# Optimization experiments

Hardware: AMD Instinct MI355X
Metric: run time of the kernel (lower is better)

Reference implementation:

```python
import jax, jax.numpy as jnp
import numpy as np

NUM_HEADS = 16
EMB = 1024
HEAD = 64
SEQ = 2048
BATCH = 4


def setup_inputs() -> dict:
    key = jax.random.key(0)
    ks = jax.random.split(key, 6)
    s = EMB ** -0.5
    x = jax.random.normal(ks[0], (BATCH, SEQ, EMB), dtype=jnp.float32)
    # per-head projection weights stacked: [H, E, D] (Linear(emb, head, bias=False) per head)
    Wq = jax.random.normal(ks[1], (NUM_HEADS, EMB, HEAD), dtype=jnp.float32) * s
    Wk = jax.random.normal(ks[2], (NUM_HEADS, EMB, HEAD), dtype=jnp.float32) * s
    Wv = jax.random.normal(ks[3], (NUM_HEADS, EMB, HEAD), dtype=jnp.float32) * s
    # output projection Linear(head*num_heads, emb): weight [E, H*D], bias [E]
    Wo = jax.random.normal(ks[4], (EMB, NUM_HEADS * HEAD), dtype=jnp.float32) * ((NUM_HEADS * HEAD) ** -0.5)
    bo = jax.random.normal(ks[5], (EMB,), dtype=jnp.float32) * 0.01
    return {"x": x, "Wq": Wq, "Wk": Wk, "Wv": Wv, "Wo": Wo, "bo": bo}


def reference(x, Wq, Wk, Wv, Wo, bo):
    B, S, E = x.shape
    scale = HEAD ** -0.5
    # batched per-head projections: [B, H, S, D]
    q = jnp.einsum('bse,hed->bhsd', x, Wq)
    k = jnp.einsum('bse,hed->bhsd', x, Wk)
    v = jnp.einsum('bse,hed->bhsd', x, Wv)
    scores = jnp.einsum('bhqd,bhkd->bhqk', q, k) * scale
    causal = jnp.tril(jnp.ones((S, S), dtype=bool))
    scores = jnp.where(causal, scores, jnp.finfo(scores.dtype).min)
    attn = jax.nn.softmax(scores, axis=-1)  # dropout disabled (eval/deterministic)
    ctx = jnp.einsum('bhqk,bhkd->bhqd', attn, v)
    # concat heads along last dim (head-major order, matching torch.cat)
    concat = ctx.transpose(0, 2, 1, 3).reshape(B, S, NUM_HEADS * HEAD)
    out = concat @ Wo.T + bo
    return out
```

## Files before the change

kernel.cpp:

```cpp
#include <hip/hip_runtime.h>

#define NHEADS 16
#define EMB 1024
#define HDIM 64
#define SEQ 2048
#define BATCH 4

typedef unsigned short u16;
typedef __attribute__((ext_vector_type(8))) __bf16 bf16x8;
typedef __attribute__((ext_vector_type(4))) float f32x4;

#if __has_builtin(__builtin_amdgcn_exp2f)
#define EXP2(x) __builtin_amdgcn_exp2f(x)
#else
#define EXP2(x) __expf((x)*0.69314718056f)
#endif
#define CL2E 0.18033688011112042f

#define BARRIER() __builtin_amdgcn_s_barrier()
#define SB0() __builtin_amdgcn_sched_barrier(0)
#define PRIO1() __builtin_amdgcn_s_setprio(1)
#define PRIO0() __builtin_amdgcn_s_setprio(0)
#define VMCNT(n) asm volatile("s_waitcnt vmcnt(" #n ")" ::: "memory")
#define LGKM0() asm volatile("s_waitcnt lgkmcnt(0)" ::: "memory")

__device__ __forceinline__ u16 f2bf(float f) {
  union { float f; unsigned u; } v; v.f = f;
  unsigned r = v.u + 0x7fffu + ((v.u >> 16) & 1u);
  return (u16)(r >> 16);
}
__device__ __forceinline__ unsigned pk2bf(float a, float b) {
  union { __bf16 h[2]; unsigned u; } x;
  x.h[0] = (__bf16)a; x.h[1] = (__bf16)b; return x.u;
}
__device__ __forceinline__ void gl16(const void* g, void* l) {
  __builtin_amdgcn_global_load_lds(
      (const __attribute__((address_space(1))) unsigned*)g,
      (__attribute__((address_space(3))) unsigned*)l, 16, 0, 0);
}
__device__ __forceinline__ unsigned PKLO(unsigned a, unsigned b) {
  return __builtin_amdgcn_perm(a, b, 0x01000504u);
}
__device__ __forceinline__ unsigned PKHI(unsigned a, unsigned b) {
  return __builtin_amdgcn_perm(a, b, 0x03020706u);
}

__global__ __launch_bounds__(256) void k_cvt(const float* __restrict__ in,
                                             u16* __restrict__ out, int n4) {
  int i = blockIdx.x * 256 + threadIdx.x;
  if (i >= n4) return;
  f32x4 v = *(const f32x4*)(in + (size_t)i * 4);
  uint2 o;
  o.x = (unsigned)f2bf(v[0]) | ((unsigned)f2bf(v[1]) << 16);
  o.y = (unsigned)f2bf(v[2]) | ((unsigned)f2bf(v[3]) << 16);
  *(uint2*)(out + (size_t)i * 4) = o;
}

__global__ __launch_bounds__(256) void k_packw(const float* __restrict__ Wq,
                                               const float* __restrict__ Wk,
                                               const float* __restrict__ Wv,
                                               u16* __restrict__ Wt) {
  const int mh = blockIdx.x;
  const int e0 = blockIdx.y * 64;
  const int mtx = mh >> 4, h = mh & 15;
  const float* W = (mtx == 0 ? Wq : (mtx == 1 ? Wk : Wv)) + (size_t)h * EMB * HDIM;
  __shared__ u16 sT[64][65];
  const int t = threadIdx.x;
  {
    int e = t >> 2, d0 = (t & 3) * 16;
#pragma unroll
    for (int jj = 0; jj < 4; jj++) {
      f32x4 v = *(const f32x4*)(W + (size_t)(e0 + e) * HDIM + d0 + jj * 4);
#pragma unroll
      for (int kk = 0; kk < 4; kk++) sT[e][d0 + jj * 4 + kk] = f2bf(v[kk]);
    }
  }
  __syncthreads();
  {
    int d = t >> 2, eb = (t & 3) * 16;
#pragma unroll
    for (int j = 0; j < 16; j++)
      Wt[(size_t)(mh * 64 + d) * EMB + e0 + eb + j] = sT[eb + j][d];
  }
}

__global__ __launch_bounds__(512, 2) void k_gemm_qkv8(const u16* __restrict__ Xb,
                                                      const u16* __restrict__ Wt,
                                                      u16* __restrict__ Q,
                                                      u16* __restrict__ K,
                                                      u16* __restrict__ V) {
  extern __shared__ __align__(16) char smem[];
  const int bid = blockIdx.x;
  const int l = (bid & 7) * 64 + (bid >> 3);
  const int mt = l & 31, nt = l >> 5;
  const int m0 = mt * 256, n0 = nt * 192;

  const int t = threadIdx.x;
  const int wave = t >> 6, lane = t & 63, lr = lane & 15, lg = lane >> 4;
  const int wr = (wave >> 2) * 128;
  const int wc = (wave & 3) * 48;

  const f32x4 fz = {0.f, 0.f, 0.f, 0.f};
  f32x4 acc[8][3];
#pragma unroll
  for (int i = 0; i < 8; i++)
#pragma unroll
    for (int j = 0; j < 3; j++) acc[i][j] = fz;

  bf16x8 af[4][2], bfr[3][2];

  auto SROUND = [&](char* ldsbase, int rbase, const u16* src, int gRowBase, int kt) {
    int rs = rbase + wave * 8;
    int row = rs + (lane >> 3);
    int gc = (lane & 7) ^ (row & 7);
    gl16(src + (size_t)(gRowBase + row) * EMB + kt * 64 + gc * 8, ldsbase + rs * 128);
  };
  auto STAGE7 = [&](char* nA, char* nB, int kt) {
    SROUND(nB, 0, Wt, n0, kt); SROUND(nB, 64, Wt, n0, kt); SROUND(nB, 128, Wt, n0, kt);
    SROUND(nA, 0, Xb, m0, kt); SROUND(nA, 64, Xb, m0, kt);
    SROUND(nA, 128, Xb, m0, kt); SROUND(nA, 192, Xb, m0, kt);
  };
  auto LOADA = [&](const char* bA, int mh) {
#pragma unroll
    for (int mf = 0; mf < 4; mf++)
#pragma unroll
      for (int kf = 0; kf < 2; kf++) {
        int row = wr + mh * 64 + mf * 16 + lr;
        af[mf][kf] = *(const bf16x8*)(bA + row * 128 + ((kf * 64 + lg * 16) ^ ((row & 7) << 4)));
      }
  };
  auto LOADB = [&](const char* bB) {
#pragma unroll
    for (int nf = 0; nf < 3; nf++)
#pragma unroll
      for (int kf = 0; kf < 2; kf++) {
        int row = wc + nf * 16 + lr;
        bfr[nf][kf] = *(const bf16x8*)(bB + row * 128 + ((kf * 64 + lg * 16) ^ ((row & 7) << 4)));
      }
  };

#define MFMAPH(MH)                                                                         \
  do {                                                                                     \
    _Pragma("unroll") for (int kf = 0; kf < 2; kf++)                                       \
    _Pragma("unroll") for (int mf = 0; mf < 4; mf++)                                       \
    _Pragma("unroll") for (int nf = 0; nf < 3; nf++)                                       \
      acc[(MH)*4 + mf][nf] = __builtin_amdgcn_mfma_f32_16x16x32_bf16(                      \
          af[mf][kf], bfr[nf][kf], acc[(MH)*4 + mf][nf], 0, 0, 0);                         \
  } while (0)

  const int NT = EMB / 64;
  STAGE7(smem, smem + 32768, 0);
  VMCNT(0);
  BARRIER();

  for (int tt = 0; tt < NT - 1; tt++) {
    const int cb = tt & 1, nb = cb ^ 1;
    char* bA = smem + cb * 57344;
    char* bB = bA + 32768;
    char* nA = smem + nb * 57344;
    char* nB = nA + 32768;
    STAGE7(nA, nB, tt + 1);
    VMCNT(7);
    BARRIER(); SB0();
    LOADA(bA, 0);
    LOADB(bB);
    PRIO1(); MFMAPH(0); PRIO0();
    LOADA(bA, 1);
    PRIO1(); MFMAPH(1); PRIO0();
    BARRIER();
  }
  {
    char* bA = smem + ((NT - 1) & 1) * 57344;
    char* bB = bA + 32768;
    VMCNT(0);
    BARRIER(); SB0();
    LOADA(bA, 0);
    LOADB(bB);
    PRIO1(); MFMAPH(0); PRIO0();
    LOADA(bA, 1);
    PRIO1(); MFMAPH(1); PRIO0();
  }
#undef MFMAPH

  const int b = m0 >> 11;
  const int s0 = m0 & 2047;
#pragma unroll
  for (int am = 0; am < 8; am++)
#pragma unroll
    for (int nf = 0; nf < 3; nf++)
#pragma unroll
      for (int r = 0; r < 4; r++) {
        int row = wr + am * 16 + lg * 4 + r;
        int n = n0 + wc + nf * 16 + lr;
        int mtx = n >> 10, h = (n >> 6) & 15, d = n & 63;
        u16* dst = (mtx == 0 ? Q : (mtx == 1 ? K : V));
        dst[((size_t)(b * NHEADS + h) * SEQ + s0 + row) * HDIM + d] = f2bf(acc[am][nf][r]);
      }
}

__global__ __launch_bounds__(256, 3) void k_attn(const u16* __restrict__ Q,
                                                 const u16* __restrict__ K,
                                                 const u16* __restrict__ V,
                                                 u16* __restrict__ Cc) {
  const int bh = blockIdx.x;
  const int qt = 15 - (int)blockIdx.y;
  const int b = bh >> 4, h = bh & 15;
  const int t = threadIdx.x;
  const int wq = t >> 6, lane = t & 63, lr = lane & 15, lg = lane >> 4;
  const size_t base = (size_t)bh * SEQ * HDIM;

  __shared__ __align__(16) char sK[2][64 * 128];
  __shared__ __align__(16) char sV[2][64 * 128];
  __shared__ __align__(16) char sP[128 * 128];

  const int kvb = (t & 15) * 4, db = (t >> 4) * 4;
  uint2 v0, v1, v2, v3;
  auto VLOAD = [&](int k0) {
    const u16* vp = V + base + (size_t)(k0 + kvb) * HDIM + db;
    v0 = *(const uint2*)(vp);
    v1 = *(const uint2*)(vp + HDIM);
    v2 = *(const uint2*)(vp + 2 * HDIM);
    v3 = *(const uint2*)(vp + 3 * HDIM);
  };
  auto VWRITE = [&](char* sv) {
    uint2 w0 = {PKLO(v0.x, v1.x), PKLO(v2.x, v3.x)};
    uint2 w1 = {PKHI(v0.x, v1.x), PKHI(v2.x, v3.x)};
    uint2 w2 = {PKLO(v0.y, v1.y), PKLO(v2.y, v3.y)};
    uint2 w3 = {PKHI(v0.y, v1.y), PKHI(v2.y, v3.y)};
    *(uint2*)(sv + (db + 0) * 128 + ((kvb * 2) ^ (((db + 0) & 7) << 4))) = w0;
    *(uint2*)(sv + (db + 1) * 128 + ((kvb * 2) ^ (((db + 1) & 7) << 4))) = w1;
    *(uint2*)(sv + (db + 2) * 128 + ((kvb * 2) ^ (((db + 2) & 7) << 4))) = w2;
    *(uint2*)(sv + (db + 3) * 128 + ((kvb * 2) ^ (((db + 3) & 7) << 4))) = w3;
  };
  auto KSTAGE = [&](char* sk, int k0) {
#pragma unroll
    for (int i = 0; i < 2; i++) {
      int rb = wq * 16 + i * 8;
      int row = rb + (lane >> 3);
      int gc = (lane & 7) ^ (row & 7);
      gl16(K + base + (size_t)(k0 + row) * HDIM + gc * 8, sk + rb * 128);
    }
  };

#pragma unroll
  for (int i = 0; i < 4; i++) {
    int rb = wq * 32 + i * 8;
    int row = rb + (lane >> 3);
    int gc = (lane & 7) ^ (row & 7);
    gl16(Q + base + (size_t)(qt * 128 + row) * HDIM + gc * 8, sP + rb * 128);
  }
  KSTAGE(sK[0], 0);
  VLOAD(0);
  VMCNT(0);
  VWRITE(sV[0]);
  __syncthreads();

  bf16x8 qf[2][2];
#pragma unroll
  for (int q2 = 0; q2 < 2; q2++)
#pragma unroll
    for (int kf = 0; kf < 2; kf++) {
      int row = wq * 32 + q2 * 16 + lr;
      qf[q2][kf] = *(const bf16x8*)(sP + row * 128 + ((kf * 64 + lg * 16) ^ ((row & 7) << 4)));
    }

  const f32x4 fz = {0.f, 0.f, 0.f, 0.f};
  f32x4 ot[4][2];
#pragma unroll
  for (int df = 0; df < 4; df++)
#pragma unroll
    for (int q2 = 0; q2 < 2; q2++) ot[df][q2] = fz;
  float m_[2] = {-1e30f, -1e30f}, l_[2] = {0.f, 0.f};

  const int nsteps = 2 * qt + 2;
  for (int step = 0; step < nsteps; step++) {
    const int k0 = step * 64;
    const int cur = step & 1, nxt = cur ^ 1;
    const bool pf = (step + 1 < nsteps);
    if (pf) {
      KSTAGE(sK[nxt], k0 + 64);
      VLOAD(k0 + 64);
    }

    f32x4 st[4][2];
#pragma unroll
    for (int kvf = 0; kvf < 4; kvf++)
#pragma unroll
      for (int q2 = 0; q2 < 2; q2++) st[kvf][q2] = fz;
#pragma unroll
    for (int kf = 0; kf < 2; kf++) {
      bf16x8 kfr[4];
#pragma unroll
      for (int kvf = 0; kvf < 4; kvf++) {
        int row = kvf * 16 + lr;
        kfr[kvf] = *(const bf16x8*)(sK[cur] + row * 128 + ((kf * 64 + lg * 16) ^ ((row & 7) << 4)));
      }
      PRIO1();
#pragma unroll
      for (int kvf = 0; kvf < 4; kvf++)
#pragma unroll
        for (int q2 = 0; q2 < 2; q2++)
          st[kvf][q2] = __builtin_amdgcn_mfma_f32_16x16x32_bf16(kfr[kvf], qf[q2][kf], st[kvf][q2], 0, 0, 0);
      PRIO0();
    }

    const bool diag = (k0 >= qt * 128);
    float mxv[2];
#pragma unroll
    for (int q2 = 0; q2 < 2; q2++) {
      if (diag) {
        const int qg = qt * 128 + wq * 32 + q2 * 16 + lr;
#pragma unroll
        for (int kvf = 0; kvf < 4; kvf++)
#pragma unroll
          for (int r = 0; r < 4; r++)
            if (k0 + kvf * 16 + 4 * lg + r > qg) st[kvf][q2][r] = -3e38f;
      }
      float mx = -3e38f;
#pragma unroll
      for (int kvf = 0; kvf < 4; kvf++)
        mx = fmaxf(mx, fmaxf(fmaxf(st[kvf][q2][0], st[kvf][q2][1]),
                             fmaxf(st[kvf][q2][2], st[kvf][q2][3])));
      mx = fmaxf(mx, __shfl_xor(mx, 16));
      mx = fmaxf(mx, __shfl_xor(mx, 32));
      mxv[q2] = mx;
    }
    if (!__all((mxv[0] <= m_[0] + 64.f) && (mxv[1] <= m_[1] + 64.f))) {
#pragma unroll
      for (int q2 = 0; q2 < 2; q2++) {
        float mnew = fmaxf(m_[q2], mxv[q2]);
        float alpha = EXP2((m_[q2] - mnew) * CL2E);
        m_[q2] = mnew;
        l_[q2] *= alpha;
#pragma unroll
        for (int df = 0; df < 4; df++) ot[df][q2] *= alpha;
      }
    }
#pragma unroll
    for (int q2 = 0; q2 < 2; q2++) {
      float nmc = -m_[q2] * CL2E;
      float rs = 0.f;
      const int prow = wq * 32 + q2 * 16 + lr;
#pragma unroll
      for (int kvf = 0; kvf < 4; kvf++) {
        float p0 = EXP2(fmaf(st[kvf][q2][0], CL2E, nmc));
        float p1 = EXP2(fmaf(st[kvf][q2][1], CL2E, nmc));
        float p2 = EXP2(fmaf(st[kvf][q2][2], CL2E, nmc));
        float p3 = EXP2(fmaf(st[kvf][q2][3], CL2E, nmc));
        rs += (p0 + p1) + (p2 + p3);
        uint2 w;
        w.x = pk2bf(p0, p1);
        w.y = pk2bf(p2, p3);
        *(uint2*)(sP + prow * 128 + ((kvf * 32 + lg * 8) ^ ((prow & 7) << 4))) = w;
      }
      rs += __shfl_xor(rs, 16);
      rs += __shfl_xor(rs, 32);
      l_[q2] += rs;
    }

#pragma unroll
    for (int kf = 0; kf < 2; kf++) {
      bf16x8 pfg[2], vf[4];
#pragma unroll
      for (int q2 = 0; q2 < 2; q2++) {
        int row = wq * 32 + q2 * 16 + lr;
        pfg[q2] = *(const bf16x8*)(sP + row * 128 + ((kf * 64 + lg * 16) ^ ((row & 7) << 4)));
      }
#pragma unroll
      for (int df = 0; df < 4; df++) {
        int row = df * 16 + lr;
        vf[df] = *(const bf16x8*)(sV[cur] + row * 128 + ((kf * 64 + lg * 16) ^ ((row & 7) << 4)));
      }
      PRIO1();
#pragma unroll
      for (int df = 0; df < 4; df++)
#pragma unroll
        for (int q2 = 0; q2 < 2; q2++)
          ot[df][q2] = __builtin_amdgcn_mfma_f32_16x16x32_bf16(vf[df], pfg[q2], ot[df][q2], 0, 0, 0);
      PRIO0();
    }

    if (pf) {
      VMCNT(0);
      VWRITE(sV[nxt]);
      LGKM0();
      BARRIER();
    }
  }

#pragma unroll
  for (int q2 = 0; q2 < 2; q2++) {
    float inv = 1.0f / l_[q2];
    int s = qt * 128 + wq * 32 + q2 * 16 + lr;
#pragma unroll
    for (int df = 0; df < 4; df++) {
      uint2 w;
      w.x = pk2bf(ot[df][q2][0] * inv, ot[df][q2][1] * inv);
      w.y = pk2bf(ot[df][q2][2] * inv, ot[df][q2][3] * inv);
      *(uint2*)(Cc + ((size_t)b * SEQ + s) * (NHEADS * HDIM) + h * HDIM + df * 16 + 4 * lg) = w;
    }
  }
}

__global__ __launch_bounds__(512, 2) void k_gemm_out8(const u16* __restrict__ Cc,
                                                      const u16* __restrict__ Wob,
                                                      const float* __restrict__ bo,
                                                      float* __restrict__ out) {
  extern __shared__ __align__(16) char smem[];
  const int bid = blockIdx.x;
  const int l = (bid & 7) * 32 + (bid >> 3);
  const int mt = l & 31, nt = l >> 5;
  const int m0 = mt * 256, n0 = nt * 128;

  const int t = threadIdx.x;
  const int wave = t >> 6, lane = t & 63, lr = lane & 15, lg = lane >> 4;
  const int wr = (wave >> 2) * 128;
  const int wc = (wave & 3) * 32;

  const f32x4 fz = {0.f, 0.f, 0.f, 0.f};
  f32x4 acc[8][2];
#pragma unroll
  for (int i = 0; i < 8; i++)
#pragma unroll
    for (int j = 0; j < 2; j++) acc[i][j] = fz;

  bf16x8 af[4][2], bfr[2][2];

  auto SROUND = [&](char* ldsbase, int rbase, const u16* src, int gRowBase, int kt) {
    int rs = rbase + wave * 8;
    int row = rs + (lane >> 3);
    int gc = (lane & 7) ^ (row & 7);
    gl16(src + (size_t)(gRowBase + row) * EMB + kt * 64 + gc * 8, ldsbase + rs * 128);
  };
  auto STAGE6 = [&](char* nA, char* nB, int kt) {
    SROUND(nB, 0, Wob, n0, kt); SROUND(nB, 64, Wob, n0, kt);
    SROUND(nA, 0, Cc, m0, kt); SROUND(nA, 64, Cc, m0, kt);
    SROUND(nA, 128, Cc, m0, kt); SROUND(nA, 192, Cc, m0, kt);
  };
  auto LOADA = [&](const char* bA, int mh) {
#pragma unroll
    for (int mf = 0; mf < 4; mf++)
#pragma unroll
      for (int kf = 0; kf < 2; kf++) {
        int row = wr + mh * 64 + mf * 16 + lr;
        af[mf][kf] = *(const bf16x8*)(bA + row * 128 + ((kf * 64 + lg * 16) ^ ((row & 7) << 4)));
      }
  };
  auto LOADB = [&](const char* bB) {
#pragma unroll
    for (int nf = 0; nf < 2; nf++)
#pragma unroll
      for (int kf = 0; kf < 2; kf++) {
        int row = wc + nf * 16 + lr;
        bfr[nf][kf] = *(const bf16x8*)(bB + row * 128 + ((kf * 64 + lg * 16) ^ ((row & 7) << 4)));
      }
  };

#define MFMAPH2(MH)                                                                        \
  do {                                                                                     \
    _Pragma("unroll") for (int kf = 0; kf < 2; kf++)                                       \
    _Pragma("unroll") for (int mf = 0; mf < 4; mf++)                                       \
    _Pragma("unroll") for (int nf = 0; nf < 2; nf++)                                       \
      acc[(MH)*4 + mf][nf] = __builtin_amdgcn_mfma_f32_16x16x32_bf16(                      \
          af[mf][kf], bfr[nf][kf], acc[(MH)*4 + mf][nf], 0, 0, 0);                         \
  } while (0)

  const int NT = EMB / 64;
  STAGE6(smem, smem + 32768, 0);
  VMCNT(0);
  BARRIER();

  for (int tt = 0; tt < NT - 1; tt++) {
    const int cb = tt & 1, nb = cb ^ 1;
    char* bA = smem + cb * 49152;
    char* bB = bA + 32768;
    char* nA = smem + nb * 49152;
    char* nB = nA + 32768;
    STAGE6(nA, nB, tt + 1);
    VMCNT(6);
    BARRIER(); SB0();
    LOADA(bA, 0);
    LOADB(bB);
    PRIO1(); MFMAPH2(0); PRIO0();
    LOADA(bA, 1);
    PRIO1(); MFMAPH2(1); PRIO0();
    BARRIER();
  }
  {
    char* bA = smem + ((NT - 1) & 1) * 49152;
    char* bB = bA + 32768;
    VMCNT(0);
    BARRIER(); SB0();
    LOADA(bA, 0);
    LOADB(bB);
    PRIO1(); MFMAPH2(0); PRIO0();
    LOADA(bA, 1);
    PRIO1(); MFMAPH2(1); PRIO0();
  }
#undef MFMAPH2

  float bv[2];
#pragma unroll
  for (int nf = 0; nf < 2; nf++) bv[nf] = bo[n0 + wc + nf * 16 + lr];
#pragma unroll
  for (int am = 0; am < 8; am++)
#pragma unroll
    for (int nf = 0; nf < 2; nf++)
#pragma unroll
      for (int r = 0; r < 4; r++) {
        int row = wr + am * 16 + lg * 4 + r;
        int n = n0 + wc + nf * 16 + lr;
        out[(size_t)(m0 + row) * EMB + n] = acc[am][nf][r] + bv[nf];
      }
}

extern "C" void kernel_launch(void* const* d_in, const int* in_sizes, int n_in,
                              void* d_out, int out_size, void* d_ws, size_t ws_size,
                              hipStream_t stream) {
  const float* x  = (const float*)d_in[0];
  const float* Wq = (const float*)d_in[1];
  const float* Wk = (const float*)d_in[2];
  const float* Wv = (const float*)d_in[3];
  const float* Wo = (const float*)d_in[4];
  const float* bo = (const float*)d_in[5];
  float* out = (float*)d_out;

  char* ws = (char*)d_ws;
  const size_t SZ_XB  = (size_t)8192 * 1024 * 2;
  const size_t SZ_WT  = (size_t)3072 * 1024 * 2;
  const size_t SZ_WOB = (size_t)1024 * 1024 * 2;
  const size_t SZ_QKV = (size_t)64 * 2048 * 64 * 2;
  u16* Xb  = (u16*)(ws);
  u16* Wt  = (u16*)(ws + SZ_XB);
  u16* Wob = (u16*)(ws + SZ_XB + SZ_WT);
  u16* Qb  = (u16*)(ws + SZ_XB + SZ_WT + SZ_WOB);
  u16* Kb  = (u16*)(ws + SZ_XB + SZ_WT + SZ_WOB + SZ_QKV);
  u16* Vb  = (u16*)(ws + SZ_XB + SZ_WT + SZ_WOB + 2 * SZ_QKV);
  u16* Cc  = (u16*)(ws + SZ_XB + SZ_WT + SZ_WOB + 3 * SZ_QKV);

  k_cvt<<<8192, 256, 0, stream>>>(x, Xb, 2097152);
  k_cvt<<<1024, 256, 0, stream>>>(Wo, Wob, 262144);
  k_packw<<<dim3(48, 16), 256, 0, stream>>>(Wq, Wk, Wv, Wt);
  k_gemm_qkv8<<<512, 512, 114688, stream>>>(Xb, Wt, Qb, Kb, Vb);
  k_attn<<<dim3(64, 16), 256, 0, stream>>>(Qb, Kb, Vb, Cc);
  k_gemm_out8<<<256, 512, 98304, stream>>>(Cc, Wob, bo, out);
}
```

Measured before the change: 166.6 us.

## Merge conversion kernels into one prep launch and interleave QKV GEMM loads with MFMA

The three preprocessing kernels (x convert, Wo convert, QKV weight pack/transpose) are merged into a single launch with a block-index dispatch, removing two kernel launches and their tail gaps. The QKV GEMM main loop is restructured: instead of issuing all seven global-to-LDS loads up front and then doing all LDS reads and MFMAs, it splits the k-tile into four quarter phases. Each phase interleaves one or two global prefetch rounds with a smaller LDS fragment load and 12 MFMAs, separated by barriers. This lowers register pressure for fragments and spreads memory issue across compute, at the cost of more barriers per iteration.

After: 164.9 us. No clear change (-1.0%).

```diff
diff --git a/kernel.cpp b/kernel.cpp
--- a/kernel.cpp
+++ b/kernel.cpp
@@ -45,42 +45,53 @@
   return __builtin_amdgcn_perm(a, b, 0x03020706u);
 }
 
-__global__ __launch_bounds__(256) void k_cvt(const float* __restrict__ in,
-                                             u16* __restrict__ out, int n4) {
-  int i = blockIdx.x * 256 + threadIdx.x;
-  if (i >= n4) return;
-  f32x4 v = *(const f32x4*)(in + (size_t)i * 4);
-  uint2 o;
-  o.x = (unsigned)f2bf(v[0]) | ((unsigned)f2bf(v[1]) << 16);
-  o.y = (unsigned)f2bf(v[2]) | ((unsigned)f2bf(v[3]) << 16);
-  *(uint2*)(out + (size_t)i * 4) = o;
-}
-
-__global__ __launch_bounds__(256) void k_packw(const float* __restrict__ Wq,
-                                               const float* __restrict__ Wk,
-                                               const float* __restrict__ Wv,
-                                               u16* __restrict__ Wt) {
-  const int mh = blockIdx.x;
-  const int e0 = blockIdx.y * 64;
-  const int mtx = mh >> 4, h = mh & 15;
-  const float* W = (mtx == 0 ? Wq : (mtx == 1 ? Wk : Wv)) + (size_t)h * EMB * HDIM;
+__global__ __launch_bounds__(256) void k_prep(const float* __restrict__ x,
+                                              const float* __restrict__ Wo,
+                                              const float* __restrict__ Wq,
+                                              const float* __restrict__ Wk,
+                                              const float* __restrict__ Wv,
+                                              u16* __restrict__ Xb,
+                                              u16* __restrict__ Wob,
+                                              u16* __restrict__ Wt) {
   __shared__ u16 sT[64][65];
+  const int bid = blockIdx.x;
   const int t = threadIdx.x;
-  {
-    int e = t >> 2, d0 = (t & 3) * 16;
-#pragma unroll
-    for (int jj = 0; jj < 4; jj++) {
-      f32x4 v = *(const f32x4*)(W + (size_t)(e0 + e) * HDIM + d0 + jj * 4);
-#pragma unroll
-      for (int kk = 0; kk < 4; kk++) sT[e][d0 + jj * 4 + kk] = f2bf(v[kk]);
-    }
-  }
-  __syncthreads();
-  {
-    int d = t >> 2, eb = (t & 3) * 16;
-#pragma unroll
-    for (int j = 0; j < 16; j++)
-      Wt[(size_t)(mh * 64 + d) * EMB + e0 + eb + j] = sT[eb + j][d];
+  if (bid < 8192) {
+    int i = bid * 256 + t;
+    f32x4 v = *(const f32x4*)(x + (size_t)i * 4);
+    uint2 o;
+    o.x = (unsigned)f2bf(v[0]) | ((unsigned)f2bf(v[1]) << 16);
+    o.y = (unsigned)f2bf(v[2]) | ((unsigned)f2bf(v[3]) << 16);
+    *(uint2*)(Xb + (size_t)i * 4) = o;
+  } else if (bid < 9216) {
+    int i = (bid - 8192) * 256 + t;
+    f32x4 v = *(const f32x4*)(Wo + (size_t)i * 4);
+    uint2 o;
+    o.x = (unsigned)f2bf(v[0]) | ((unsigned)f2bf(v[1]) << 16);
+    o.y = (unsigned)f2bf(v[2]) | ((unsigned)f2bf(v[3]) << 16);
+    *(uint2*)(Wob + (size_t)i * 4) = o;
+  } else {
+    int pb = bid - 9216;
+    const int mh = pb % 48;
+    const int e0 = (pb / 48) * 64;
+    const int mtx = mh >> 4, h = mh & 15;
+    const float* W = (mtx == 0 ? Wq : (mtx == 1 ? Wk : Wv)) + (size_t)h * EMB * HDIM;
+    {
+      int e = t >> 2, d0 = (t & 3) * 16;
+#pragma unroll
+      for (int jj = 0; jj < 4; jj++) {
+        f32x4 v = *(const f32x4*)(W + (size_t)(e0 + e) * HDIM + d0 + jj * 4);
+#pragma unroll
+        for (int kk = 0; kk < 4; kk++) sT[e][d0 + jj * 4 + kk] = f2bf(v[kk]);
+      }
+    }
+    __syncthreads();
+    {
+      int d = t >> 2, eb = (t & 3) * 16;
+#pragma unroll
+      for (int j = 0; j < 16; j++)
+        Wt[(size_t)(mh * 64 + d) * EMB + e0 + eb + j] = sT[eb + j][d];
+    }
   }
 }
 
@@ -107,7 +118,7 @@
 #pragma unroll
     for (int j = 0; j < 3; j++) acc[i][j] = fz;
 
-  bf16x8 af[4][2], bfr[3][2];
+  bf16x8 af[4], bfr0[3], bfr1[3];
 
   auto SROUND = [&](char* ldsbase, int rbase, const u16* src, int gRowBase, int kt) {
     int rs = rbase + wave * 8;
@@ -115,41 +126,39 @@
     int gc = (lane & 7) ^ (row & 7);
     gl16(src + (size_t)(gRowBase + row) * EMB + kt * 64 + gc * 8, ldsbase + rs * 128);
   };
-  auto STAGE7 = [&](char* nA, char* nB, int kt) {
-    SROUND(nB, 0, Wt, n0, kt); SROUND(nB, 64, Wt, n0, kt); SROUND(nB, 128, Wt, n0, kt);
-    SROUND(nA, 0, Xb, m0, kt); SROUND(nA, 64, Xb, m0, kt);
-    SROUND(nA, 128, Xb, m0, kt); SROUND(nA, 192, Xb, m0, kt);
-  };
-  auto LOADA = [&](const char* bA, int mh) {
-#pragma unroll
-    for (int mf = 0; mf < 4; mf++)
-#pragma unroll
-      for (int kf = 0; kf < 2; kf++) {
-        int row = wr + mh * 64 + mf * 16 + lr;
-        af[mf][kf] = *(const bf16x8*)(bA + row * 128 + ((kf * 64 + lg * 16) ^ ((row & 7) << 4)));
-      }
-  };
-  auto LOADB = [&](const char* bB) {
-#pragma unroll
-    for (int nf = 0; nf < 3; nf++)
-#pragma unroll
-      for (int kf = 0; kf < 2; kf++) {
-        int row = wc + nf * 16 + lr;
-        bfr[nf][kf] = *(const bf16x8*)(bB + row * 128 + ((kf * 64 + lg * 16) ^ ((row & 7) << 4)));
-      }
-  };
-
-#define MFMAPH(MH)                                                                         \
+  auto LOADA4 = [&](const char* bA, int mh, int kf) {
+#pragma unroll
+    for (int mf = 0; mf < 4; mf++) {
+      int row = wr + mh * 64 + mf * 16 + lr;
+      af[mf] = *(const bf16x8*)(bA + row * 128 + ((kf * 64 + lg * 16) ^ ((row & 7) << 4)));
+    }
+  };
+  auto LOADB3 = [&](const char* bB, int kf, bf16x8* b3) {
+#pragma unroll
+    for (int nf = 0; nf < 3; nf++) {
+      int row = wc + nf * 16 + lr;
+      b3[nf] = *(const bf16x8*)(bB + row * 128 + ((kf * 64 + lg * 16) ^ ((row & 7) << 4)));
+    }
+  };
+
+#define MFMA12(MH, BF)                                                                     \
   do {                                                                                     \
-    _Pragma("unroll") for (int kf = 0; kf < 2; kf++)                                       \
+    PRIO1();                                                                               \
     _Pragma("unroll") for (int mf = 0; mf < 4; mf++)                                       \
     _Pragma("unroll") for (int nf = 0; nf < 3; nf++)                                       \
       acc[(MH)*4 + mf][nf] = __builtin_amdgcn_mfma_f32_16x16x32_bf16(                      \
-          af[mf][kf], bfr[nf][kf], acc[(MH)*4 + mf][nf], 0, 0, 0);                         \
+          af[mf], BF[nf], acc[(MH)*4 + mf][nf], 0, 0, 0);                                  \
+    PRIO0();                                                                               \
   } while (0)
 
   const int NT = EMB / 64;
-  STAGE7(smem, smem + 32768, 0);
+  {
+    char* nA = smem;
+    char* nB = smem + 32768;
+    SROUND(nB, 0, Wt, n0, 0); SROUND(nB, 64, Wt, n0, 0); SROUND(nB, 128, Wt, n0, 0);
+    SROUND(nA, 0, Xb, m0, 0); SROUND(nA, 64, Xb, m0, 0);
+    SROUND(nA, 128, Xb, m0, 0); SROUND(nA, 192, Xb, m0, 0);
+  }
   VMCNT(0);
   BARRIER();
 
@@ -159,14 +168,28 @@
     char* bB = bA + 32768;
     char* nA = smem + nb * 57344;
     char* nB = nA + 32768;
-    STAGE7(nA, nB, tt + 1);
-    VMCNT(7);
+    SROUND(nB, 0, Wt, n0, tt + 1);
+    SROUND(nB, 64, Wt, n0, tt + 1);
+    VMCNT(2);
     BARRIER(); SB0();
-    LOADA(bA, 0);
-    LOADB(bB);
-    PRIO1(); MFMAPH(0); PRIO0();
-    LOADA(bA, 1);
-    PRIO1(); MFMAPH(1); PRIO0();
+    LOADB3(bB, 0, bfr0);
+    LOADA4(bA, 0, 0);
+    MFMA12(0, bfr0);
+    BARRIER();
+    SROUND(nB, 128, Wt, n0, tt + 1);
+    SROUND(nA, 0, Xb, m0, tt + 1);
+    LOADA4(bA, 1, 0);
+    MFMA12(1, bfr0);
+    BARRIER();
+    SROUND(nA, 64, Xb, m0, tt + 1);
+    SROUND(nA, 128, Xb, m0, tt + 1);
+    LOADB3(bB, 1, bfr1);
+    LOADA4(bA, 0, 1);
+    MFMA12(0, bfr1);
+    BARRIER();
+    SROUND(nA, 192, Xb, m0, tt + 1);
+    LOADA4(bA, 1, 1);
+    MFMA12(1, bfr1);
     BARRIER();
   }
   {
@@ -174,13 +197,18 @@
     char* bB = bA + 32768;
     VMCNT(0);
     BARRIER(); SB0();
-    LOADA(bA, 0);
-    LOADB(bB);
-    PRIO1(); MFMAPH(0); PRIO0();
-    LOADA(bA, 1);
-    PRIO1(); MFMAPH(1); PRIO0();
-  }
-#undef MFMAPH
+    LOADB3(bB, 0, bfr0);
+    LOADA4(bA, 0, 0);
+    MFMA12(0, bfr0);
+    LOADA4(bA, 1, 0);
+    MFMA12(1, bfr0);
+    LOADB3(bB, 1, bfr1);
+    LOADA4(bA, 0, 1);
+    MFMA12(0, bfr1);
+    LOADA4(bA, 1, 1);
+    MFMA12(1, bfr1);
+  }
+#undef MFMA12
 
   const int b = m0 >> 11;
   const int s0 = m0 & 2047;
@@ -538,9 +566,7 @@
   u16* Vb  = (u16*)(ws + SZ_XB + SZ_WT + SZ_WOB + 2 * SZ_QKV);
   u16* Cc  = (u16*)(ws + SZ_XB + SZ_WT + SZ_WOB + 3 * SZ_QKV);
 
-  k_cvt<<<8192, 256, 0, stream>>>(x, Xb, 2097152);
-  k_cvt<<<1024, 256, 0, stream>>>(Wo, Wob, 262144);
-  k_packw<<<dim3(48, 16), 256, 0, stream>>>(Wq, Wk, Wv, Wt);
+  k_prep<<<9984, 256, 0, stream>>>(x, Wo, Wq, Wk, Wv, Xb, Wob, Wt);
   k_gemm_qkv8<<<512, 512, 114688, stream>>>(Xb, Wt, Qb, Kb, Vb);
   k_attn<<<dim3(64, 16), 256, 0, stream>>>(Qb, Kb, Vb, Cc);
   k_gemm_out8<<<256, 512, 98304, stream>>>(Cc, Wob, bo, out);
```
